# Kernel tuning notes

Hardware: AMD Instinct MI355X
Metric: run time of the kernel (lower is better)

## Reference

```python
import jax, jax.numpy as jnp
import numpy as np

EPS = 1e-6
FEAT = 1024
HEADS = 16
HDIM = FEAT // HEADS
FF = 500


def setup_inputs() -> dict:
    key = jax.random.key(0)
    ks = jax.random.split(key, 12)
    B, S = 4, 2048
    inp = {
        "x": jax.random.normal(ks[0], (B, S, FEAT), jnp.float32),
        "mask": jax.random.randint(ks[1], (B, S, S), 0, 2, jnp.int32),
        "alpha1": jnp.ones((FEAT,), jnp.float32),
        "bias1": jnp.zeros((FEAT,), jnp.float32),
        "alpha2": jnp.ones((FEAT,), jnp.float32),
        "bias2": jnp.zeros((FEAT,), jnp.float32),
        "Wq": jax.random.normal(ks[2], (FEAT, FEAT), jnp.float32) * (1.0 / np.sqrt(FEAT)),
        "bq": jnp.zeros((FEAT,), jnp.float32),
        "Wk": jax.random.normal(ks[3], (FEAT, FEAT), jnp.float32) * (1.0 / np.sqrt(FEAT)),
        "bk": jnp.zeros((FEAT,), jnp.float32),
        "Wv": jax.random.normal(ks[4], (FEAT, FEAT), jnp.float32) * (1.0 / np.sqrt(FEAT)),
        "bv": jnp.zeros((FEAT,), jnp.float32),
        "Wo": jax.random.normal(ks[5], (FEAT, FEAT), jnp.float32) * (1.0 / np.sqrt(FEAT)),
        "bo": jnp.zeros((FEAT,), jnp.float32),
        "W1": jax.random.normal(ks[6], (FEAT, FF), jnp.float32) * (1.0 / np.sqrt(FEAT)),
        "b1": jnp.zeros((FF,), jnp.float32),
        "W2": jax.random.normal(ks[7], (FF, FEAT), jnp.float32) * (1.0 / np.sqrt(FF)),
        "b2": jnp.zeros((FEAT,), jnp.float32),
    }
    return inp


def _norm(x, alpha, bias):
    m = jnp.mean(x, axis=-1, keepdims=True)
    # torch.std uses Bessel's correction (ddof=1)
    s = jnp.std(x, axis=-1, keepdims=True, ddof=1)
    return alpha * (x - m) / (s + EPS) + bias


def _attn(x2, mask, Wq, bq, Wk, bk, Wv, bv, Wo, bo):
    B, S, _ = x2.shape
    q = (x2 @ Wq + bq).reshape(B, S, HEADS, HDIM)
    k = (x2 @ Wk + bk).reshape(B, S, HEADS, HDIM)
    v = (x2 @ Wv + bv).reshape(B, S, HEADS, HDIM)
    scores = jnp.einsum("bqhd,bkhd->bhqk", q, k) / np.sqrt(HDIM).astype(np.float32)
    # faithful to source: masked positions filled with -1e-09 (not -1e9)
    scores = jnp.where(mask[:, None, :, :] == 0, jnp.float32(-1e-09), scores)
    probs = jax.nn.softmax(scores, axis=-1)
    out = jnp.einsum("bhqk,bkhd->bqhd", probs, v).reshape(B, S, FEAT)
    return out @ Wo + bo


def reference(x, mask, alpha1, bias1, alpha2, bias2, Wq, bq, Wk, bk, Wv, bv, Wo, bo, W1, b1, W2, b2):
    x2 = _norm(x, alpha1, bias1)
    x = x + _attn(x2, mask, Wq, bq, Wk, bk, Wv, bv, Wo, bo)
    x2 = _norm(x, alpha2, bias2)
    h = jax.nn.elu(x2 @ W1 + b1)
    x = x + (h @ W2 + b2)
    return x
```

## Files before the change

### kernel.cpp

```cpp
#include <hip/hip_runtime.h>
#include <hip/hip_bf16.h>
#include <math.h>

#define BATCH 4
#define SEQ 2048
#define FEAT 1024
#define HEADS 16
#define HDIM 64
#define FF 500
#define FFP 512
#define ROWS (BATCH * SEQ)
#define QKVSTR 3072
#define AQ 128

typedef unsigned short ushortT;
typedef __attribute__((ext_vector_type(8))) short short8;
typedef __attribute__((ext_vector_type(4))) float floatx4;

#if defined(__has_builtin) && __has_builtin(__builtin_amdgcn_exp2f)
#define EXP2F(x) __builtin_amdgcn_exp2f(x)
#else
#define EXP2F(x) exp2f(x)
#endif

__device__ __forceinline__ unsigned short f2bf(float f) {
    unsigned int u = __builtin_bit_cast(unsigned int, f);
    u += 0x7fffu + ((u >> 16) & 1u);
    return (unsigned short)(u >> 16);
}
__device__ __forceinline__ float bf2f(short b) {
    unsigned int u = ((unsigned int)(unsigned short)b) << 16;
    return __builtin_bit_cast(float, u);
}

__device__ __forceinline__ void async16(void* lds, const void* g) {
    __builtin_amdgcn_global_load_lds(
        (const __attribute__((address_space(1))) unsigned int*)g,
        (__attribute__((address_space(3))) unsigned int*)lds, 16, 0, 0);
}

__global__ void prep_kernel(const float* __restrict__ Wq, const float* __restrict__ Wk,
                            const float* __restrict__ Wv, const float* __restrict__ Wo,
                            const float* __restrict__ W1, const float* __restrict__ W2,
                            const float* __restrict__ bq, const float* __restrict__ bk,
                            const float* __restrict__ bv, const float* __restrict__ b1,
                            ushortT* __restrict__ Wqkvt, ushortT* __restrict__ Wot,
                            ushortT* __restrict__ W1t, ushortT* __restrict__ W2t,
                            float* __restrict__ bqkv, float* __restrict__ b1p)
{
    const int t = blockIdx.x;
    const int tid = threadIdx.x;
    if (t == 1280) {
        for (int i = tid; i < QKVSTR; i += 256)
            bqkv[i] = (i < 1024) ? bq[i] : ((i < 2048) ? bk[i - 1024] : bv[i - 2048]);
        for (int i = tid; i < FFP; i += 256)
            b1p[i] = (i < FF) ? b1[i] : 0.0f;
        return;
    }
    const float* W; ushortT* Wt; int K, N, Kp, bx, by;
    if (t < 1024) {
        const int wi = t >> 8, lt = t & 255;
        bx = lt & 15; by = lt >> 4; K = FEAT; N = FEAT; Kp = FEAT;
        W  = (wi == 0) ? Wq : (wi == 1) ? Wk : (wi == 2) ? Wv : Wo;
        Wt = (wi == 3) ? Wot : (Wqkvt + (size_t)wi * FEAT * FEAT);
    } else if (t < 1152) {
        const int lt = t - 1024; bx = lt & 7; by = lt >> 3;
        K = FEAT; N = FF; Kp = FEAT; W = W1; Wt = W1t;
    } else {
        const int lt = t - 1152; bx = lt & 15; by = lt >> 4;
        K = FF; N = FEAT; Kp = FFP; W = W2; Wt = W2t;
    }

    __shared__ float T[64][65];
    const int n0 = bx * 64, k0 = by * 64;
    const int r = tid >> 4;
    const int c = (tid & 15) * 4;
    #pragma unroll
    for (int i = 0; i < 4; i++) {
        const int kk = k0 + r + i * 16;
        #pragma unroll
        for (int e = 0; e < 4; e++) {
            const int nn = n0 + c + e;
            T[r + i * 16][c + e] = (kk < K && nn < N) ? W[(size_t)kk * N + nn] : 0.0f;
        }
    }
    __syncthreads();
    #pragma unroll
    for (int i = 0; i < 4; i++) {
        const int nn = r + i * 16;
        ushort4 o;
        o.x = f2bf(T[c + 0][nn]);
        o.y = f2bf(T[c + 1][nn]);
        o.z = f2bf(T[c + 2][nn]);
        o.w = f2bf(T[c + 3][nn]);
        *(ushort4*)(Wt + (size_t)(n0 + nn) * Kp + k0 + c) = o;
    }
}

__global__ void maskbits_kernel(const int* __restrict__ mask,
                                unsigned int* __restrict__ bits)
{
    const int lane = threadIdx.x & 63;
    const size_t stride = (size_t)gridDim.x * 256;
    const size_t total = (size_t)BATCH * SEQ * SEQ;
    for (size_t g = (size_t)blockIdx.x * 256 + threadIdx.x; g < total; g += stride) {
        const unsigned long long bal = __ballot(mask[g] != 0);
        if (lane == 0)  bits[g >> 5] = (unsigned int)bal;
        if (lane == 32) bits[g >> 5] = (unsigned int)(bal >> 32);
    }
}

__global__ void ln_kernel(const float* __restrict__ x,
                          const float* __restrict__ alpha,
                          const float* __restrict__ bias,
                          ushortT* __restrict__ out)
{
    __shared__ float p1[4], p2[4];
    const int row = blockIdx.x;
    const int tid = threadIdx.x;
    const int wave = tid >> 6, lane = tid & 63;
    float4 v = ((const float4*)(x + (size_t)row * FEAT))[tid];

    float s1 = v.x + v.y + v.z + v.w;
    float s2 = v.x * v.x + v.y * v.y + v.z * v.z + v.w * v.w;
    #pragma unroll
    for (int off = 32; off > 0; off >>= 1) {
        s1 += __shfl_xor(s1, off);
        s2 += __shfl_xor(s2, off);
    }
    if (lane == 0) { p1[wave] = s1; p2[wave] = s2; }
    __syncthreads();
    const float t1 = p1[0] + p1[1] + p1[2] + p1[3];
    const float t2 = p2[0] + p2[1] + p2[2] + p2[3];
    const float mean = t1 * (1.0f / 1024.0f);
    const float var = fmaxf(t2 - 1024.0f * mean * mean, 0.0f) * (1.0f / 1023.0f);
    const float inv = 1.0f / (sqrtf(var) + 1e-6f);

    const float4 a = ((const float4*)alpha)[tid];
    const float4 b = ((const float4*)bias)[tid];
    ushort4 o;
    o.x = f2bf(a.x * (v.x - mean) * inv + b.x);
    o.y = f2bf(a.y * (v.y - mean) * inv + b.y);
    o.z = f2bf(a.z * (v.z - mean) * inv + b.z);
    o.w = f2bf(a.w * (v.w - mean) * inv + b.w);
    ((ushort4*)(out + (size_t)row * FEAT))[tid] = o;
}

template<int ACT, int RES, int OUT_BF16, int BN, int VSPLIT>
__global__ __launch_bounds__(256)
void mfma_gemm(const ushortT* __restrict__ A, const ushortT* __restrict__ Bt,
               const float* __restrict__ bias, const float* __restrict__ R,
               void* __restrict__ Cout, ushortT* __restrict__ Vt,
               int M, int N, int K)
{
    constexpr int MT = (BN == 128) ? 4 : 2;
    constexpr int MSPAN = (BN == 128) ? 64 : 32;
    __shared__ ushortT As[2][128 * 32];
    __shared__ ushortT Bs[2][BN * 32];

    const int tid  = threadIdx.x;
    const int wave = tid >> 6, lane = tid & 63;
    const int quad = lane >> 4, l16 = lane & 15;
    const int wm = (BN == 128) ? (wave >> 1) : wave;
    const int wn = (BN == 128) ? (wave & 1) : 0;

    const int nbx = gridDim.x;
    int lid = blockIdx.y * nbx + blockIdx.x;
    const int cpx = (nbx * gridDim.y) >> 3;
    lid = (lid & 7) * cpx + (lid >> 3);
    const int row0 = (lid / nbx) * 128, col0 = (lid % nbx) * BN;

    const floatx4 z4 = {0.f, 0.f, 0.f, 0.f};
    floatx4 acc[MT][4];
    #pragma unroll
    for (int i = 0; i < MT; i++)
        #pragma unroll
        for (int j = 0; j < 4; j++) acc[i][j] = z4;

    for (int k0 = 0; k0 < K; k0 += 64) {
        __syncthreads();
        #pragma unroll
        for (int kh = 0; kh < 2; kh++) {
            #pragma unroll
            for (int i = 0; i < 2; i++) {
                const int rbase = 16 * (wave + 4 * i);
                const int r = rbase + (lane >> 2);
                const int co = (lane & 3) * 8;
                async16((char*)As[kh] + rbase * 64,
                        A + (size_t)(row0 + r) * K + k0 + kh * 32 + co);
            }
            if (BN == 128) {
                #pragma unroll
                for (int i = 0; i < 2; i++) {
                    const int rbase = 16 * (wave + 4 * i);
                    const int r = rbase + (lane >> 2);
                    const int co = (lane & 3) * 8;
                    async16((char*)Bs[kh] + rbase * 64,
                            Bt + (size_t)(col0 + r) * K + k0 + kh * 32 + co);
                }
            } else {
                const int rbase = 16 * wave;
                const int r = rbase + (lane >> 2);
                const int co = (lane & 3) * 8;
                async16((char*)Bs[kh] + rbase * 64,
                        Bt + (size_t)(col0 + r) * K + k0 + kh * 32 + co);
            }
        }
        __syncthreads();

        #pragma unroll
        for (int kh = 0; kh < 2; kh++) {
            short8 af[MT], bf[4];
            #pragma unroll
            for (int mt = 0; mt < MT; mt++)
                af[mt] = *(const short8*)&As[kh][(MSPAN * wm + 16 * mt + l16) * 32 + quad * 8];
            #pragma unroll
            for (int nt = 0; nt < 4; nt++)
                bf[nt] = *(const short8*)&Bs[kh][(64 * wn + 16 * nt + l16) * 32 + quad * 8];
            #pragma unroll
            for (int mt = 0; mt < MT; mt++)
                #pragma unroll
                for (int nt = 0; nt < 4; nt++)
                    acc[mt][nt] = __builtin_amdgcn_mfma_f32_16x16x32_bf16(
                        af[mt], bf[nt], acc[mt][nt], 0, 0, 0);
        }
    }

    #pragma unroll
    for (int mt = 0; mt < MT; mt++) {
        #pragma unroll
        for (int nt = 0; nt < 4; nt++) {
            const int col = col0 + 64 * wn + 16 * nt + l16;
            const int rbase = row0 + MSPAN * wm + 16 * mt + quad * 4;
            if (VSPLIT && col >= 2048) {
                const int bb = rbase >> 11;
                const int jj = rbase & 2047;
                const float bv = bias[col];
                ushort4 o4;
                o4.x = f2bf(acc[mt][nt][0] + bv);
                o4.y = f2bf(acc[mt][nt][1] + bv);
                o4.z = f2bf(acc[mt][nt][2] + bv);
                o4.w = f2bf(acc[mt][nt][3] + bv);
                *(ushort4*)(Vt + ((size_t)(bb * 1024 + (col - 2048))) * SEQ + jj) = o4;
                continue;
            }
            #pragma unroll
            for (int r = 0; r < 4; r++) {
                const int row = rbase + r;
                float val = acc[mt][nt][r] + bias[col];
                if (ACT == 1) val = (val > 0.0f) ? val : (__expf(val) - 1.0f);
                if (RES) val += R[(size_t)row * N + col];
                if (OUT_BF16)
                    ((ushortT*)Cout)[(size_t)row * N + col] = f2bf(val);
                else
                    ((float*)Cout)[(size_t)row * N + col] = val;
            }
        }
    }
}

__global__ __launch_bounds__(512)
void mfma_attn(const ushortT* __restrict__ qkv, const ushortT* __restrict__ vt,
               const unsigned int* __restrict__ mbits, ushortT* __restrict__ attn_out)
{
    __shared__ ushortT Ks[2][64 * 64];
    __shared__ ushortT Vts[2][64 * 64];
    __shared__ ushortT Ps[AQ * 64];

    const int tid = threadIdx.x;
    const int wave = tid >> 6, lane = tid & 63;
    const int quad = lane >> 4, l16 = lane & 15;
    const int bid = ((blockIdx.x & 7) << 7) | (blockIdx.x >> 3);
    const int qt = bid & 15, h = (bid >> 4) & 15, b = bid >> 8;
    const int q0 = qt * AQ;

    const ushortT* qptr = qkv;
    const ushortT* kptr = qkv + 1024;

    short8 qf[2];
    {
        const size_t qrow = (size_t)(b * SEQ + q0 + 16 * wave + l16);
        short8 t0 = *(const short8*)(qptr + qrow * QKVSTR + h * 64 + quad * 8);
        short8 t1 = *(const short8*)(qptr + qrow * QKVSTR + h * 64 + 32 + quad * 8);
        const float cs = 0.125f * 1.4426950408889634f;
        #pragma unroll
        for (int i = 0; i < 8; i++) {
            qf[0][i] = (short)f2bf(bf2f(t0[i]) * cs);
            qf[1][i] = (short)f2bf(bf2f(t1[i]) * cs);
        }
    }

    short8 ones8;
    #pragma unroll
    for (int i = 0; i < 8; i++) ones8[i] = (short)0x3F80;

    const floatx4 z4 = {0.f, 0.f, 0.f, 0.f};
    floatx4 o[4];
    #pragma unroll
    for (int dt = 0; dt < 4; dt++) o[dt] = z4;
    floatx4 lacc = z4;

    const int rr = tid >> 3;
    const int c0 = tid & 7;
    const ushortT* gk = kptr + (size_t)(b * SEQ + rr) * QKVSTR + h * 64 + c0 * 8;
    const ushortT* gv = vt + ((size_t)((b * HEADS + h) * 64 + rr)) * SEQ + c0 * 8;
    short8 rk, rv;

#define ATTN_ISSUE() {                                                       \
    rk = *(const short8*)gk;                                                 \
    rv = *(const short8*)gv;                                                 \
    gk += (size_t)64 * QKVSTR; gv += 64; }

#define ATTN_WRITE(BI) {                                                     \
    *(short8*)&Ks[BI][rr * 64 + ((c0 ^ (rr & 7)) * 8)] = rk;                 \
    *(short8*)&Vts[BI][rr * 64 + ((c0 ^ (rr & 7)) * 8)] = rv; }

    const unsigned int* mrowp =
        mbits + (size_t)(b * SEQ + q0 + 16 * wave + l16) * (SEQ / 32);
    const int mloc = 16 * wave + l16;

    ATTN_ISSUE();
    ATTN_WRITE(0);
    unsigned int w0 = mrowp[0], w1 = mrowp[1];

    #pragma unroll 2
    for (int jt = 0; jt < 32; jt++) {
        __syncthreads();
        const int cur = jt & 1;
        unsigned int wn0 = 0, wn1 = 0;
        if (jt < 31) {
            ATTN_ISSUE();
            wn0 = mrowp[jt * 2 + 2];
            wn1 = mrowp[jt * 2 + 3];
        }

        floatx4 st[4];
        __builtin_amdgcn_s_setprio(1);
        #pragma unroll
        for (int nt = 0; nt < 4; nt++) {
            const int j = nt * 16 + l16;
            short8 ka0 = *(const short8*)&Ks[cur][j * 64 + ((quad ^ (j & 7)) * 8)];
            short8 ka1 = *(const short8*)&Ks[cur][j * 64 + (((4 + quad) ^ (j & 7)) * 8)];
            floatx4 t = z4;
            t = __builtin_amdgcn_mfma_f32_16x16x32_bf16(ka0, qf[0], t, 0, 0, 0);
            t = __builtin_amdgcn_mfma_f32_16x16x32_bf16(ka1, qf[1], t, 0, 0, 0);
            st[nt] = t;
        }
        __builtin_amdgcn_s_setprio(0);

        #pragma unroll
        for (int nt = 0; nt < 4; nt++) {
            const unsigned int ww = (nt & 2) ? w1 : w0;
            const unsigned int wsh = ww >> ((nt & 1) * 16 + quad * 4);
            float p[4];
            p[0] = EXP2F((wsh & 1u) ? st[nt][0] : 0.0f);
            p[1] = EXP2F((wsh & 2u) ? st[nt][1] : 0.0f);
            p[2] = EXP2F((wsh & 4u) ? st[nt][2] : 0.0f);
            p[3] = EXP2F((wsh & 8u) ? st[nt][3] : 0.0f);
            const int j0 = nt * 16 + quad * 4;
            const int chunk = (j0 >> 3) ^ (mloc & 7);
            const int ci = j0 & 7;
            ushortT* dst = &Ps[mloc * 64 + chunk * 8 + ci];
            *(__hip_bfloat162*)(dst)     = __float22bfloat162_rn(make_float2(p[0], p[1]));
            *(__hip_bfloat162*)(dst + 2) = __float22bfloat162_rn(make_float2(p[2], p[3]));
        }

        short8 pa0 = *(const short8*)&Ps[mloc * 64 + ((quad ^ (mloc & 7)) * 8)];
        short8 pa1 = *(const short8*)&Ps[mloc * 64 + (((4 + quad) ^ (mloc & 7)) * 8)];
        lacc = __builtin_amdgcn_mfma_f32_16x16x32_bf16(pa0, ones8, lacc, 0, 0, 0);
        lacc = __builtin_amdgcn_mfma_f32_16x16x32_bf16(pa1, ones8, lacc, 0, 0, 0);
        __builtin_amdgcn_s_setprio(1);
        #pragma unroll
        for (int dt = 0; dt < 4; dt++) {
            const int d = dt * 16 + l16;
            short8 vb0 = *(const short8*)&Vts[cur][d * 64 + ((quad ^ (d & 7)) * 8)];
            short8 vb1 = *(const short8*)&Vts[cur][d * 64 + (((4 + quad) ^ (d & 7)) * 8)];
            o[dt] = __builtin_amdgcn_mfma_f32_16x16x32_bf16(pa0, vb0, o[dt], 0, 0, 0);
            o[dt] = __builtin_amdgcn_mfma_f32_16x16x32_bf16(pa1, vb1, o[dt], 0, 0, 0);
        }
        __builtin_amdgcn_s_setprio(0);

        if (jt < 31) {
            ATTN_WRITE(cur ^ 1);
            w0 = wn0; w1 = wn1;
        }
    }

    #pragma unroll
    for (int r = 0; r < 4; r++) {
        const float inv_l = 1.0f / lacc[r];
        const size_t row = (size_t)(b * SEQ + q0 + 16 * wave + quad * 4 + r);
        #pragma unroll
        for (int dt = 0; dt < 4; dt++) {
            attn_out[row * FEAT + h * 64 + dt * 16 + l16] = f2bf(o[dt][r] * inv_l);
        }
    }
#undef ATTN_ISSUE
#undef ATTN_WRITE
}

extern "C" void kernel_launch(void* const* d_in, const int* in_sizes, int n_in,
                              void* d_out, int out_size, void* d_ws, size_t ws_size,
                              hipStream_t stream)
{
    const float* x      = (const float*)d_in[0];
    const int*   mask   = (const int*)d_in[1];
    const float* alpha1 = (const float*)d_in[2];
    const float* bias1  = (const float*)d_in[3];
    const float* alpha2 = (const float*)d_in[4];
    const float* bias2  = (const float*)d_in[5];
    const float* Wq     = (const float*)d_in[6];
    const float* bq     = (const float*)d_in[7];
    const float* Wk     = (const float*)d_in[8];
    const float* bk     = (const float*)d_in[9];
    const float* Wv     = (const float*)d_in[10];
    const float* bv     = (const float*)d_in[11];
    const float* Wo     = (const float*)d_in[12];
    const float* bo     = (const float*)d_in[13];
    const float* W1     = (const float*)d_in[14];
    const float* b1     = (const float*)d_in[15];
    const float* W2     = (const float*)d_in[16];
    const float* b2     = (const float*)d_in[17];
    float* out = (float*)d_out;

    char* ws = (char*)d_ws;
    const size_t MB = 1024 * 1024;
    ushortT* x2b    = (ushortT*)(ws);
    ushortT* attn_o = (ushortT*)(ws);
    ushortT* qkv    = (ushortT*)(ws + 16 * MB);
    ushortT* x2b2   = (ushortT*)(ws + 16 * MB);
    ushortT* hbuf   = (ushortT*)(ws + 32 * MB);
    ushortT* vtb    = (ushortT*)(ws + 64 * MB);
    ushortT* Wqkvt  = (ushortT*)(ws + 80 * MB);
    ushortT* Wot    = (ushortT*)(ws + 86 * MB);
    ushortT* W1t    = (ushortT*)(ws + 88 * MB);
    ushortT* W2t    = (ushortT*)(ws + 89 * MB);
    float*   b1p    = (float*)  (ws + 90 * MB);
    float*   bqkv   = (float*)  (ws + 90 * MB + 16384);
    unsigned int* mbits = (unsigned int*)(ws + 91 * MB);

    const dim3 blk(256);

    prep_kernel<<<1281, blk, 0, stream>>>(Wq, Wk, Wv, Wo, W1, W2, bq, bk, bv, b1,
                                          Wqkvt, Wot, W1t, W2t, bqkv, b1p);
    maskbits_kernel<<<2048, blk, 0, stream>>>(mask, mbits);

    ln_kernel<<<ROWS, blk, 0, stream>>>(x, alpha1, bias1, x2b);

    mfma_gemm<0, 0, 1, 128, 1><<<dim3(24, 64), blk, 0, stream>>>(
        x2b, Wqkvt, bqkv, nullptr, qkv, vtb, ROWS, QKVSTR, FEAT);

    mfma_attn<<<BATCH * HEADS * (SEQ / AQ), dim3(512), 0, stream>>>(qkv, vtb, mbits, attn_o);

    mfma_gemm<0, 1, 0, 128, 0><<<dim3(8, 64), blk, 0, stream>>>(
        attn_o, Wot, bo, x, out, nullptr, ROWS, FEAT, FEAT);

    ln_kernel<<<ROWS, blk, 0, stream>>>(out, alpha2, bias2, x2b2);

    mfma_gemm<1, 0, 1, 64, 0><<<dim3(FFP / 64, 64), blk, 0, stream>>>(
        x2b2, W1t, b1p, nullptr, hbuf, nullptr, ROWS, FFP, FEAT);

    mfma_gemm<0, 1, 0, 128, 0><<<dim3(8, 64), blk, 0, stream>>>(
        hbuf, W2t, b2, out, out, nullptr, ROWS, FEAT, FFP);
}
```

Baseline: 437.3 us.

## Double-buffer GEMM K-loop to prefetch next slice during MFMA compute

Restructures the bf16 GEMM main loop from loading two 32-wide K halves and then computing, into a ping-pong pipeline. The next 32-wide slice is issued asynchronously into the alternate LDS buffer before the current slice is multiplied. This is meant to overlap global-to-LDS transfer latency with MFMA work and to drop the second barrier per step. It relies on the barrier's implicit wait on outstanding async loads for correctness. Each iteration now carries less compute to hide latency behind.

```diff
diff --git a/kernel.cpp b/kernel.cpp
--- a/kernel.cpp
+++ b/kernel.cpp
@@ -177,54 +177,52 @@
         #pragma unroll
         for (int j = 0; j < 4; j++) acc[i][j] = z4;
 
-    for (int k0 = 0; k0 < K; k0 += 64) {
+    const int sr = lane >> 2;
+    const int sco = (lane & 3) * 8;
+
+#define STAGE(P, KO) {                                                        \
+    _Pragma("unroll")                                                         \
+    for (int i = 0; i < 2; i++) {                                             \
+        const int rbase = 16 * (wave + 4 * i);                                \
+        async16((char*)As[P] + rbase * 64,                                    \
+                A + (size_t)(row0 + rbase + sr) * K + (KO) + sco);            \
+    }                                                                         \
+    if (BN == 128) {                                                          \
+        _Pragma("unroll")                                                     \
+        for (int i = 0; i < 2; i++) {                                         \
+            const int rbase = 16 * (wave + 4 * i);                            \
+            async16((char*)Bs[P] + rbase * 64,                                \
+                    Bt + (size_t)(col0 + rbase + sr) * K + (KO) + sco);       \
+        }                                                                     \
+    } else {                                                                  \
+        const int rbase = 16 * wave;                                          \
+        async16((char*)Bs[P] + rbase * 64,                                    \
+                Bt + (size_t)(col0 + rbase + sr) * K + (KO) + sco);           \
+    } }
+
+    const int NK = K >> 5;
+    STAGE(0, 0);
+
+    for (int ks = 0; ks < NK; ks++) {
         __syncthreads();
-        #pragma unroll
-        for (int kh = 0; kh < 2; kh++) {
-            #pragma unroll
-            for (int i = 0; i < 2; i++) {
-                const int rbase = 16 * (wave + 4 * i);
-                const int r = rbase + (lane >> 2);
-                const int co = (lane & 3) * 8;
-                async16((char*)As[kh] + rbase * 64,
-                        A + (size_t)(row0 + r) * K + k0 + kh * 32 + co);
-            }
-            if (BN == 128) {
-                #pragma unroll
-                for (int i = 0; i < 2; i++) {
-                    const int rbase = 16 * (wave + 4 * i);
-                    const int r = rbase + (lane >> 2);
-                    const int co = (lane & 3) * 8;
-                    async16((char*)Bs[kh] + rbase * 64,
-                            Bt + (size_t)(col0 + r) * K + k0 + kh * 32 + co);
-                }
-            } else {
-                const int rbase = 16 * wave;
-                const int r = rbase + (lane >> 2);
-                const int co = (lane & 3) * 8;
-                async16((char*)Bs[kh] + rbase * 64,
-                        Bt + (size_t)(col0 + r) * K + k0 + kh * 32 + co);
-            }
-        }
-        __syncthreads();
-
-        #pragma unroll
-        for (int kh = 0; kh < 2; kh++) {
-            short8 af[MT], bf[4];
-            #pragma unroll
-            for (int mt = 0; mt < MT; mt++)
-                af[mt] = *(const short8*)&As[kh][(MSPAN * wm + 16 * mt + l16) * 32 + quad * 8];
+        if (ks + 1 < NK) STAGE((ks + 1) & 1, (ks + 1) << 5);
+
+        const int p = ks & 1;
+        short8 af[MT], bf4[4];
+        #pragma unroll
+        for (int mt = 0; mt < MT; mt++)
+            af[mt] = *(const short8*)&As[p][(MSPAN * wm + 16 * mt + l16) * 32 + quad * 8];
+        #pragma unroll
+        for (int nt = 0; nt < 4; nt++)
+            bf4[nt] = *(const short8*)&Bs[p][(64 * wn + 16 * nt + l16) * 32 + quad * 8];
+        #pragma unroll
+        for (int mt = 0; mt < MT; mt++)
             #pragma unroll
             for (int nt = 0; nt < 4; nt++)
-                bf[nt] = *(const short8*)&Bs[kh][(64 * wn + 16 * nt + l16) * 32 + quad * 8];
-            #pragma unroll
-            for (int mt = 0; mt < MT; mt++)
-                #pragma unroll
-                for (int nt = 0; nt < 4; nt++)
-                    acc[mt][nt] = __builtin_amdgcn_mfma_f32_16x16x32_bf16(
-                        af[mt], bf[nt], acc[mt][nt], 0, 0, 0);
-        }
-    }
+                acc[mt][nt] = __builtin_amdgcn_mfma_f32_16x16x32_bf16(
+                    af[mt], bf4[nt], acc[mt][nt], 0, 0, 0);
+    }
+#undef STAGE
 
     #pragma unroll
     for (int mt = 0; mt < MT; mt++) {
```

Result: no change. 434.8 us (-0.6%).
